# Kernel tuning notes

Hardware: AMD Instinct MI355X
Metric: run time of the kernel (lower is better)

Reference implementation:

```python
import jax, jax.numpy as jnp
import numpy as np

B, S, D, H, DH = 2, 2048, 1024, 16, 64
GLOBAL_RATIO = 0.1
LN_EPS = 1e-5


def setup_inputs() -> dict:
    key = jax.random.key(0)
    ks = jax.random.split(key, 8)
    w = lambda k, shape: jax.random.normal(k, shape, jnp.float32) * 0.02
    return {
        'x': jax.random.normal(ks[0], (B, S, D), jnp.float32),
        'Wq': w(ks[1], (D, H * DH)),
        'Wk': w(ks[2], (D, H * DH)),
        'Wv': w(ks[3], (D, H * DH)),
        'Wo': w(ks[4], (H * DH, D)),
        'bo': jnp.zeros((D,), jnp.float32),
        'ln_gamma': jnp.ones((DH,), jnp.float32),
        'ln_beta': jnp.zeros((DH,), jnp.float32),
        'Wg': w(ks[5], (2 * DH, DH)),
        'bg': jnp.zeros((DH,), jnp.float32),
    }


def _layernorm(x, gamma, beta):
    mu = jnp.mean(x, axis=-1, keepdims=True)
    var = jnp.mean(jnp.square(x - mu), axis=-1, keepdims=True)
    return (x - mu) * jax.lax.rsqrt(var + LN_EPS) * gamma + beta


def reference(x, Wq, Wk, Wv, Wo, bo, ln_gamma, ln_beta, Wg, bg):
    b, s, _ = x.shape
    # projections -> [b, h, n, d]
    split = lambda t: t.reshape(b, s, H, DH).transpose(0, 2, 1, 3)
    q = split(x @ Wq)
    k = split(x @ Wk)
    v = split(x @ Wv)
    scale = DH ** -0.5

    # local (full) attention: manual QK^T / softmax / AV
    scores = jnp.einsum('bhnd,bhmd->bhnm', q, k) * scale  # [b,h,s,s]
    attn = jax.nn.softmax(scores, axis=-1)
    local_out = jnp.einsum('bhnm,bhmd->bhnd', attn, v)

    # cross-segment fusion: top-k keys by norm per (b, h)
    num_global = max(1, int(s * GLOBAL_RATIO))
    key_norms = jnp.linalg.norm(k, axis=-1)  # [b,h,s]
    _, top_idx = jax.lax.top_k(key_norms, num_global)  # [b,h,g]
    idx = top_idx[..., None]  # [b,h,g,1]
    global_k = jnp.take_along_axis(k, idx, axis=2)  # [b,h,g,d]
    global_v = jnp.take_along_axis(v, idx, axis=2)
    g_scores = jnp.einsum('bhnd,bhgd->bhng', q, global_k) * scale
    g_attn = jax.nn.softmax(g_scores, axis=-1)
    global_out = jnp.einsum('bhng,bhgd->bhnd', g_attn, global_v)
    global_out = _layernorm(global_out, ln_gamma, ln_beta)

    # learned gate over [local, global]
    cat = jnp.concatenate([local_out, global_out], axis=-1)  # [b,h,s,2d]
    gate = jax.nn.sigmoid(cat @ Wg + bg)
    fused = gate * local_out + (1.0 - gate) * global_out

    out = fused.transpose(0, 2, 1, 3).reshape(b, s, H * DH)  # b h n d -> b n (h d)
    return out @ Wo + bo
```

## Files before the change

### kernel.cpp

```cpp
#include <hip/hip_runtime.h>


constexpr int SEQ    = 2048;
constexpr int DMODEL = 1024;
constexpr int NH     = 16;
constexpr int DHEAD  = 64;
constexpr int BHT    = 32;
constexpr int NG     = 204;
constexpr int NGPAD  = 256;
constexpr float LNEPS = 1e-5f;

typedef __attribute__((ext_vector_type(8))) short short8;
typedef __attribute__((ext_vector_type(4))) short short4v;
typedef __attribute__((ext_vector_type(4))) float f32x4;

__device__ __forceinline__ unsigned short f2bf(float f) {
    unsigned int u = __float_as_uint(f);
    u += 0x7FFFu + ((u >> 16) & 1u);
    return (unsigned short)(u >> 16);
}
__device__ __forceinline__ float bf2f(unsigned short b) {
    return __uint_as_float(((unsigned int)b) << 16);
}

__global__ __launch_bounds__(256)
void prep_k(const float* __restrict__ x,
            const float* __restrict__ Wq, const float* __restrict__ Wv,
            const float* __restrict__ Wo, const float* __restrict__ Wk,
            const float* __restrict__ Wg,
            unsigned short* __restrict__ xh, unsigned short* __restrict__ xl,
            unsigned short* __restrict__ Wqt, unsigned short* __restrict__ Wvt,
            unsigned short* __restrict__ Wot, unsigned short* __restrict__ Wkh,
            unsigned short* __restrict__ Wkl, unsigned short* __restrict__ Wgt)
{
    const int bid = blockIdx.x;
    const int tid = threadIdx.x;

    if (bid < 2048) {
        int i = (bid * 256 + tid) << 3;
        short8 h, l;
#pragma unroll
        for (int j = 0; j < 8; ++j) {
            float v = x[i + j];
            unsigned short hb = f2bf(v);
            h[j] = (short)hb;
            l[j] = (short)f2bf(v - bf2f(hb));
        }
        *(short8*)(xh + i) = h;
        *(short8*)(xl + i) = l;
        return;
    }
    if (bid == 3072) {
#pragma unroll
        for (int i = 0; i < 32; ++i) {
            int o = tid * 32 + i;
            int dg = o >> 7, jj = o & 127;
            Wgt[o] = f2bf(Wg[jj * 64 + dg]);
        }
        return;
    }

    __shared__ float tile[64][68];
    const int sub = bid - 2048;
    const int which = sub >> 8;
    const int b = sub & 255;
    const int n0 = (b & 15) * 64, k0 = (b >> 4) * 64;
    const float* W = (which == 0) ? Wq : (which == 1) ? Wv : (which == 2) ? Wo : Wk;
    const int Kd = DMODEL, Nd = DMODEL;

#pragma unroll
    for (int p = 0; p < 4; ++p) {
        int c = tid + (p << 8);
        int r = c >> 4, c4 = (c & 15) << 2;
        *(float4*)&tile[r][c4] = *(const float4*)(W + (size_t)(k0 + r) * Nd + n0 + c4);
    }
    __syncthreads();
#pragma unroll
    for (int p = 0; p < 4; ++p) {
        int c = tid + (p << 8);
        int n = c >> 4, k4 = (c & 15) << 2;
        if (which < 3) {
            unsigned short* Wt = (which == 0) ? Wqt : (which == 1) ? Wvt : Wot;
            short4v o;
#pragma unroll
            for (int j = 0; j < 4; ++j) o[j] = (short)f2bf(tile[k4 + j][n]);
            *(short4v*)(Wt + (size_t)(n0 + n) * Kd + k0 + k4) = o;
        } else {
            short4v oh, ol;
#pragma unroll
            for (int j = 0; j < 4; ++j) {
                float v = tile[k4 + j][n];
                unsigned short hb = f2bf(v);
                oh[j] = (short)hb;
                ol[j] = (short)f2bf(v - bf2f(hb));
            }
            *(short4v*)(Wkh + (size_t)(n0 + n) * Kd + k0 + k4) = oh;
            *(short4v*)(Wkl + (size_t)(n0 + n) * Kd + k0 + k4) = ol;
        }
    }
}

__global__ __launch_bounds__(512)
void gemm_bf16_k(const unsigned short* __restrict__ A,
                 const unsigned short* __restrict__ Bt,
                 const float* __restrict__ bias,
                 void* __restrict__ outv, void* __restrict__ outv2,
                 unsigned short* __restrict__ vtout,
                 int M, int N, int K, int mode)
{
    __shared__ __align__(16) unsigned short As[128][72];
    __shared__ __align__(16) unsigned short Bs[128][72];
    const int tid = threadIdx.x;
    const int lane = tid & 63, wave = tid >> 6;
    const int quad = lane >> 4, ln = lane & 15;
    const int mh = (wave >> 2) << 6;
    const int nh = (wave & 3) << 5;
    const int m0 = blockIdx.y * 128, n0 = blockIdx.x * 128;

    f32x4 acc[4][2];
#pragma unroll
    for (int i = 0; i < 4; ++i)
#pragma unroll
        for (int j = 0; j < 2; ++j) acc[i][j] = (f32x4){0.f, 0.f, 0.f, 0.f};

    short8 areg[2], breg[2];
#pragma unroll
    for (int p = 0; p < 2; ++p) {
        int c = tid + (p << 9);
        int row = c >> 3, col8 = (c & 7) << 3;
        areg[p] = *(const short8*)(A + (size_t)(m0 + row) * K + col8);
        breg[p] = *(const short8*)(Bt + (size_t)(n0 + row) * K + col8);
    }

    for (int k0 = 0; k0 < K; k0 += 64) {
        __syncthreads();
#pragma unroll
        for (int p = 0; p < 2; ++p) {
            int c = tid + (p << 9);
            int row = c >> 3, col8 = (c & 7) << 3;
            *(short8*)&As[row][col8] = areg[p];
            *(short8*)&Bs[row][col8] = breg[p];
        }
        __syncthreads();
        if (k0 + 64 < K) {
#pragma unroll
            for (int p = 0; p < 2; ++p) {
                int c = tid + (p << 9);
                int row = c >> 3, col8 = (c & 7) << 3;
                areg[p] = *(const short8*)(A + (size_t)(m0 + row) * K + k0 + 64 + col8);
                breg[p] = *(const short8*)(Bt + (size_t)(n0 + row) * K + k0 + 64 + col8);
            }
        }
#pragma unroll
        for (int ch = 0; ch < 2; ++ch) {
            short8 af[4], bf[2];
#pragma unroll
            for (int mt = 0; mt < 4; ++mt)
                af[mt] = *(const short8*)&As[mh + mt * 16 + ln][ch * 32 + quad * 8];
#pragma unroll
            for (int nt = 0; nt < 2; ++nt)
                bf[nt] = *(const short8*)&Bs[nh + nt * 16 + ln][ch * 32 + quad * 8];
#pragma unroll
            for (int mt = 0; mt < 4; ++mt)
#pragma unroll
                for (int nt = 0; nt < 2; ++nt)
                    acc[mt][nt] = __builtin_amdgcn_mfma_f32_16x16x32_bf16(
                        af[mt], bf[nt], acc[mt][nt], 0, 0, 0);
        }
    }

    if (mode == 0) {
        float* out = (float*)outv;
#pragma unroll
        for (int mt = 0; mt < 4; ++mt)
#pragma unroll
            for (int nt = 0; nt < 2; ++nt)
#pragma unroll
                for (int r = 0; r < 4; ++r) {
                    int m = m0 + mh + mt * 16 + quad * 4 + r;
                    int n = n0 + nh + nt * 16 + ln;
                    out[(size_t)m * N + n] = acc[mt][nt][r] + bias[n];
                }
    } else {
#pragma unroll
        for (int mt = 0; mt < 4; ++mt)
#pragma unroll
            for (int nt = 0; nt < 2; ++nt) {
                int n = n0 + nh + nt * 16 + ln;
                int mb = m0 + mh + mt * 16 + quad * 4;
                int b = mb >> 11, s0 = mb & (SEQ - 1);
                int d = n & 63;
                if (n < DMODEL) {
                    int h = n >> 6;
                    unsigned short* qp_ =
                        (unsigned short*)outv + ((size_t)(b * NH + h) * SEQ + s0) * DHEAD + d;
#pragma unroll
                    for (int r = 0; r < 4; ++r)
                        qp_[(size_t)r * DHEAD] = f2bf(acc[mt][nt][r] * 0.125f);
                } else {
                    int h = (n >> 6) - NH;
                    unsigned short* vp_ =
                        (unsigned short*)outv2 + ((size_t)(b * NH + h) * SEQ + s0) * DHEAD + d;
                    short4v tv;
#pragma unroll
                    for (int r = 0; r < 4; ++r) {
                        unsigned short bv = f2bf(acc[mt][nt][r]);
                        vp_[(size_t)r * DHEAD] = bv;
                        tv[r] = (short)bv;
                    }
                    *(short4v*)(vtout + ((size_t)(b * NH + h) * DHEAD + d) * SEQ + s0) = tv;
                }
            }
    }
}

__global__ __launch_bounds__(512)
void gemm_kproj_mfma(const unsigned short* __restrict__ xh,
                     const unsigned short* __restrict__ xl,
                     const unsigned short* __restrict__ Wh,
                     const unsigned short* __restrict__ Wl,
                     unsigned short* __restrict__ kout,
                     float* __restrict__ norms2)
{
    __shared__ __align__(16) unsigned short Ah[64][72];
    __shared__ __align__(16) unsigned short Al[64][72];
    __shared__ __align__(16) unsigned short Bh[128][72];
    __shared__ __align__(16) unsigned short Bl[128][72];
    const int K = DMODEL;
    const int tid = threadIdx.x;
    const int lane = tid & 63, wave = tid >> 6;
    const int quad = lane >> 4, ln = lane & 15;
    const int mh = (wave >> 1) << 4;
    const int nh = (wave & 1) << 6;
    const int m0 = blockIdx.y * 64, n0 = blockIdx.x * 128;

    f32x4 acc[4];
#pragma unroll
    for (int j = 0; j < 4; ++j) acc[j] = (f32x4){0.f, 0.f, 0.f, 0.f};

    const int arow = tid >> 3, acol8 = (tid & 7) << 3;
    short8 ahreg, alreg, bhreg[2], blreg[2];
    {
        size_t ga = (size_t)(m0 + arow) * K + acol8;
        ahreg = *(const short8*)(xh + ga);
        alreg = *(const short8*)(xl + ga);
#pragma unroll
        for (int p = 0; p < 2; ++p) {
            int c = tid + (p << 9);
            int row = c >> 3, col8 = (c & 7) << 3;
            size_t gb = (size_t)(n0 + row) * K + col8;
            bhreg[p] = *(const short8*)(Wh + gb);
            blreg[p] = *(const short8*)(Wl + gb);
        }
    }

    for (int k0 = 0; k0 < K; k0 += 64) {
        __syncthreads();
        *(short8*)&Ah[arow][acol8] = ahreg;
        *(short8*)&Al[arow][acol8] = alreg;
#pragma unroll
        for (int p = 0; p < 2; ++p) {
            int c = tid + (p << 9);
            int row = c >> 3, col8 = (c & 7) << 3;
            *(short8*)&Bh[row][col8] = bhreg[p];
            *(short8*)&Bl[row][col8] = blreg[p];
        }
        __syncthreads();
        if (k0 + 64 < K) {
            size_t ga = (size_t)(m0 + arow) * K + k0 + 64 + acol8;
            ahreg = *(const short8*)(xh + ga);
            alreg = *(const short8*)(xl + ga);
#pragma unroll
            for (int p = 0; p < 2; ++p) {
                int c = tid + (p << 9);
                int row = c >> 3, col8 = (c & 7) << 3;
                size_t gb = (size_t)(n0 + row) * K + k0 + 64 + col8;
                bhreg[p] = *(const short8*)(Wh + gb);
                blreg[p] = *(const short8*)(Wl + gb);
            }
        }
#pragma unroll
        for (int ch = 0; ch < 2; ++ch) {
            short8 bh4[4], bl4[4];
#pragma unroll
            for (int nt = 0; nt < 4; ++nt) {
                bh4[nt] = *(const short8*)&Bh[nh + nt * 16 + ln][ch * 32 + quad * 8];
                bl4[nt] = *(const short8*)&Bl[nh + nt * 16 + ln][ch * 32 + quad * 8];
            }
            short8 ah = *(const short8*)&Ah[mh + ln][ch * 32 + quad * 8];
            short8 al = *(const short8*)&Al[mh + ln][ch * 32 + quad * 8];
#pragma unroll
            for (int nt = 0; nt < 4; ++nt) {
                acc[nt] = __builtin_amdgcn_mfma_f32_16x16x32_bf16(ah, bh4[nt], acc[nt], 0, 0, 0);
                acc[nt] = __builtin_amdgcn_mfma_f32_16x16x32_bf16(ah, bl4[nt], acc[nt], 0, 0, 0);
                acc[nt] = __builtin_amdgcn_mfma_f32_16x16x32_bf16(al, bh4[nt], acc[nt], 0, 0, 0);
            }
        }
    }

    const int h = (n0 + nh) >> 6;
#pragma unroll
    for (int r = 0; r < 4; ++r) {
        int m = m0 + mh + quad * 4 + r;
        int b = m >> 11, s = m & (SEQ - 1);
        size_t rowbase = ((size_t)(b * NH + h) * SEQ + s) * DHEAD;
#pragma unroll
        for (int nt = 0; nt < 4; ++nt)
            kout[rowbase + nt * 16 + ln] = f2bf(acc[nt][r]);
        float s2 = acc[0][r] * acc[0][r] + acc[1][r] * acc[1][r] +
                   acc[2][r] * acc[2][r] + acc[3][r] * acc[3][r];
#pragma unroll
        for (int off = 1; off <= 8; off <<= 1)
            s2 += __shfl_xor(s2, off);
        if (ln == 0)
            norms2[(size_t)(b * NH + h) * SEQ + s] = s2;
    }
}

__global__ __launch_bounds__(512)
void topk_gather_k(const float* __restrict__ norms2,
                   const unsigned short* __restrict__ k,
                   const unsigned short* __restrict__ v,
                   unsigned short* __restrict__ gk,
                   unsigned short* __restrict__ gvt)
{
    __shared__ unsigned long long keys[SEQ];
    __shared__ int tix[NGPAD];
    __shared__ __align__(16) unsigned short T[64][72];
    const int bh = blockIdx.x;
    const int tid = threadIdx.x;
    const float* nb = norms2 + (size_t)bh * SEQ;
    const size_t base = (size_t)bh * SEQ * DHEAD;

    for (int i = tid; i < SEQ; i += 512) {
        float nrm = sqrtf(nb[i]);
        keys[i] = ((unsigned long long)__float_as_uint(nrm) << 32) |
                  (unsigned int)(0xFFFFFFFFu - (unsigned int)i);
    }
    __syncthreads();
    for (int kk = 2; kk <= SEQ; kk <<= 1) {
        for (int j = kk >> 1; j > 0; j >>= 1) {
            for (int i = tid; i < SEQ; i += 512) {
                int ixj = i ^ j;
                if (ixj > i) {
                    unsigned long long a = keys[i], b = keys[ixj];
                    bool up = ((i & kk) == 0);
                    if ((a > b) == up) { keys[i] = b; keys[ixj] = a; }
                }
            }
            __syncthreads();
        }
    }
    if (tid < NGPAD) {
        tix[tid] = (tid < NG)
            ? (int)(0xFFFFFFFFu - (unsigned int)(keys[SEQ - 1 - tid] & 0xFFFFFFFFu))
            : 0;
    }
    __syncthreads();

    for (int t = 0; t < NGPAD / 64; ++t) {
        {
            int idx = tid;
            int row = idx >> 3, col8 = (idx & 7) << 3;
            int g = t * 64 + row;
            short8 kv = (short8)0, vv = (short8)0;
            if (g < NG) {
                int sidx = tix[g];
                kv = *(const short8*)(k + base + (size_t)sidx * DHEAD + col8);
                vv = *(const short8*)(v + base + (size_t)sidx * DHEAD + col8);
            }
            *(short8*)(gk + ((size_t)bh * NGPAD + g) * DHEAD + col8) = kv;
            *(short8*)&T[row][col8] = vv;
        }
        __syncthreads();
        {
            int idx = tid;
            int d = idx >> 3, k8 = (idx & 7) << 3;
            short8 o;
#pragma unroll
            for (int i = 0; i < 8; ++i) o[i] = (short)T[k8 + i][d];
            *(short8*)(gvt + ((size_t)bh * DHEAD + d) * NGPAD + t * 64 + k8) = o;
        }
        __syncthreads();
    }
}

__global__ __launch_bounds__(512)
void attn_fused_k(const unsigned short* __restrict__ qb,
                  const unsigned short* __restrict__ kb,
                  const unsigned short* __restrict__ vt,
                  const unsigned short* __restrict__ gk,
                  const unsigned short* __restrict__ gvt,
                  const unsigned short* __restrict__ Wgt,
                  const float* __restrict__ gamma,
                  const float* __restrict__ beta,
                  const float* __restrict__ bg,
                  unsigned short* __restrict__ fused)
{
    __shared__ __align__(16) unsigned short Ks[64][72];
    __shared__ __align__(16) unsigned short Vt[64][72];
    __shared__ __align__(16) unsigned short Ps[128][72];
    __shared__ __align__(16) unsigned short Wgs[64][136];
    const int flat = blockIdx.x;
    const int bh = ((flat >> 7) << 3) | (flat & 7);
    const int q0 = ((flat >> 3) & 15) * 128;
    const int tid = threadIdx.x;
    const int lane = tid & 63, wave = tid >> 6;
    const int quad = lane >> 4, ln = lane & 15;
    const size_t base = (size_t)bh * SEQ * DHEAD;
    const unsigned short* gkb = gk + (size_t)bh * NGPAD * DHEAD;
    const unsigned short* gvb = gvt + (size_t)bh * DHEAD * NGPAD;

#pragma unroll
    for (int p = 0; p < 2; ++p) {
        int idx = tid + (p << 9);
        *(short8*)&Wgs[idx >> 4][(idx & 15) << 3] = *(const short8*)(Wgt + idx * 8);
    }

    short8 qf0, qf1;
    {
        const unsigned short* qp = qb + base + (size_t)(q0 + wave * 16 + ln) * DHEAD;
        qf0 = *(const short8*)(qp + quad * 8);
        qf1 = *(const short8*)(qp + 32 + quad * 8);
    }

    f32x4 O[4], Og[4];
#pragma unroll
    for (int nt = 0; nt < 4; ++nt) {
        O[nt] = (f32x4){0.f, 0.f, 0.f, 0.f};
        Og[nt] = (f32x4){0.f, 0.f, 0.f, 0.f};
    }
    float ls[4] = {0.f, 0.f, 0.f, 0.f};
    float lg[4] = {0.f, 0.f, 0.f, 0.f};

    short8 kreg = *(const short8*)(kb + base + (size_t)(tid >> 3) * DHEAD + ((tid & 7) << 3));
    short8 vreg = *(const short8*)(vt + base + (size_t)(tid >> 3) * SEQ + ((tid & 7) << 3));
    const int srow = tid >> 3, scol8 = (tid & 7) << 3;

    for (int t = 0; t < SEQ / 64; ++t) {
        __syncthreads();
        *(short8*)&Ks[srow][scol8] = kreg;
        *(short8*)&Vt[srow][scol8] = vreg;
        __syncthreads();
        if (t + 1 < SEQ / 64) {
            kreg = *(const short8*)(kb + base + (size_t)((t + 1) * 64 + srow) * DHEAD + scol8);
            vreg = *(const short8*)(vt + base + (size_t)srow * SEQ + (t + 1) * 64 + scol8);
        } else {
            kreg = *(const short8*)(gkb + (size_t)srow * DHEAD + scol8);
            vreg = *(const short8*)(gvb + (size_t)srow * NGPAD + scol8);
        }

        f32x4 s[4];
#pragma unroll
        for (int nt = 0; nt < 4; ++nt) {
            s[nt] = (f32x4){0.f, 0.f, 0.f, 0.f};
            short8 kf0 = *(const short8*)&Ks[nt * 16 + ln][quad * 8];
            short8 kf1 = *(const short8*)&Ks[nt * 16 + ln][32 + quad * 8];
            s[nt] = __builtin_amdgcn_mfma_f32_16x16x32_bf16(qf0, kf0, s[nt], 0, 0, 0);
            s[nt] = __builtin_amdgcn_mfma_f32_16x16x32_bf16(qf1, kf1, s[nt], 0, 0, 0);
        }
#pragma unroll
        for (int nt = 0; nt < 4; ++nt)
#pragma unroll
            for (int r = 0; r < 4; ++r) {
                float p = __expf(s[nt][r]);
                unsigned int us = __float_as_uint(p) >> 16;
                Ps[wave * 16 + quad * 4 + r][nt * 16 + ln] = (unsigned short)us;
                ls[r] += __uint_as_float(us << 16);
            }
#pragma unroll
        for (int ch = 0; ch < 2; ++ch) {
            short8 pf = *(const short8*)&Ps[wave * 16 + ln][ch * 32 + quad * 8];
#pragma unroll
            for (int nt = 0; nt < 4; ++nt) {
                short8 vf = *(const short8*)&Vt[nt * 16 + ln][ch * 32 + quad * 8];
                O[nt] = __builtin_amdgcn_mfma_f32_16x16x32_bf16(pf, vf, O[nt], 0, 0, 0);
            }
        }
    }

    for (int t = 0; t < NGPAD / 64; ++t) {
        __syncthreads();
        *(short8*)&Ks[srow][scol8] = kreg;
        *(short8*)&Vt[srow][scol8] = vreg;
        __syncthreads();
        if (t + 1 < NGPAD / 64) {
            kreg = *(const short8*)(gkb + (size_t)((t + 1) * 64 + srow) * DHEAD + scol8);
            vreg = *(const short8*)(gvb + (size_t)srow * NGPAD + (t + 1) * 64 + scol8);
        }

        f32x4 s[4];
#pragma unroll
        for (int nt = 0; nt < 4; ++nt) {
            s[nt] = (f32x4){0.f, 0.f, 0.f, 0.f};
            short8 kf0 = *(const short8*)&Ks[nt * 16 + ln][quad * 8];
            short8 kf1 = *(const short8*)&Ks[nt * 16 + ln][32 + quad * 8];
            s[nt] = __builtin_amdgcn_mfma_f32_16x16x32_bf16(qf0, kf0, s[nt], 0, 0, 0);
            s[nt] = __builtin_amdgcn_mfma_f32_16x16x32_bf16(qf1, kf1, s[nt], 0, 0, 0);
        }
#pragma unroll
        for (int nt = 0; nt < 4; ++nt) {
            bool valid = (t * 64 + nt * 16 + ln) < NG;
#pragma unroll
            for (int r = 0; r < 4; ++r) {
                float p = valid ? __expf(s[nt][r]) : 0.f;
                unsigned int us = __float_as_uint(p) >> 16;
                Ps[wave * 16 + quad * 4 + r][nt * 16 + ln] = (unsigned short)us;
                lg[r] += __uint_as_float(us << 16);
            }
        }
#pragma unroll
        for (int ch = 0; ch < 2; ++ch) {
            short8 pf = *(const short8*)&Ps[wave * 16 + ln][ch * 32 + quad * 8];
#pragma unroll
            for (int nt = 0; nt < 4; ++nt) {
                short8 vf = *(const short8*)&Vt[nt * 16 + ln][ch * 32 + quad * 8];
                Og[nt] = __builtin_amdgcn_mfma_f32_16x16x32_bf16(pf, vf, Og[nt], 0, 0, 0);
            }
        }
    }

#pragma unroll
    for (int off = 1; off <= 8; off <<= 1)
#pragma unroll
        for (int r = 0; r < 4; ++r) {
            ls[r] += __shfl_xor(ls[r], off);
            lg[r] += __shfl_xor(lg[r], off);
        }
    float invl[4];
#pragma unroll
    for (int r = 0; r < 4; ++r) invl[r] = 1.f / ls[r];

    float xs[4][4];
#pragma unroll
    for (int r = 0; r < 4; ++r) {
        float inv = 1.f / lg[r];
#pragma unroll
        for (int nt = 0; nt < 4; ++nt) xs[nt][r] = Og[nt][r] * inv;
    }
    float mu[4], rsd[4];
#pragma unroll
    for (int r = 0; r < 4; ++r) {
        float sm = xs[0][r] + xs[1][r] + xs[2][r] + xs[3][r];
#pragma unroll
        for (int off = 1; off <= 8; off <<= 1) sm += __shfl_xor(sm, off);
        mu[r] = sm * (1.f / 64.f);
    }
#pragma unroll
    for (int r = 0; r < 4; ++r) {
        float sv = 0.f;
#pragma unroll
        for (int nt = 0; nt < 4; ++nt) {
            float d = xs[nt][r] - mu[r];
            sv += d * d;
        }
#pragma unroll
        for (int off = 1; off <= 8; off <<= 1) sv += __shfl_xor(sv, off);
        rsd[r] = rsqrtf(sv * (1.f / 64.f) + LNEPS);
    }
#pragma unroll
    for (int nt = 0; nt < 4; ++nt) {
        float g = gamma[nt * 16 + ln], bb = beta[nt * 16 + ln];
#pragma unroll
        for (int r = 0; r < 4; ++r)
            xs[nt][r] = (xs[nt][r] - mu[r]) * rsd[r] * g + bb;
    }

    float lf[4][4];
#pragma unroll
    for (int nt = 0; nt < 4; ++nt)
#pragma unroll
        for (int r = 0; r < 4; ++r) {
            lf[nt][r] = O[nt][r] * invl[r];
            Ps[wave * 16 + quad * 4 + r][nt * 16 + ln] = f2bf(lf[nt][r]);
        }
    f32x4 gacc[4];
#pragma unroll
    for (int ng = 0; ng < 4; ++ng) {
        float bgv = bg[ng * 16 + ln];
        gacc[ng] = (f32x4){bgv, bgv, bgv, bgv};
    }
#pragma unroll
    for (int ch = 0; ch < 2; ++ch) {
        short8 af = *(const short8*)&Ps[wave * 16 + ln][ch * 32 + quad * 8];
#pragma unroll
        for (int ng = 0; ng < 4; ++ng) {
            short8 bf = *(const short8*)&Wgs[ng * 16 + ln][ch * 32 + quad * 8];
            gacc[ng] = __builtin_amdgcn_mfma_f32_16x16x32_bf16(af, bf, gacc[ng], 0, 0, 0);
        }
    }
#pragma unroll
    for (int nt = 0; nt < 4; ++nt)
#pragma unroll
        for (int r = 0; r < 4; ++r)
            Ps[wave * 16 + quad * 4 + r][nt * 16 + ln] = f2bf(xs[nt][r]);
#pragma unroll
    for (int ch = 0; ch < 2; ++ch) {
        short8 af = *(const short8*)&Ps[wave * 16 + ln][ch * 32 + quad * 8];
#pragma unroll
        for (int ng = 0; ng < 4; ++ng) {
            short8 bf = *(const short8*)&Wgs[ng * 16 + ln][64 + ch * 32 + quad * 8];
            gacc[ng] = __builtin_amdgcn_mfma_f32_16x16x32_bf16(af, bf, gacc[ng], 0, 0, 0);
        }
    }

    const int b = bh >> 4, h = bh & 15;
#pragma unroll
    for (int ng = 0; ng < 4; ++ng)
#pragma unroll
        for (int r = 0; r < 4; ++r) {
            float gt = 1.f / (1.f + __expf(-gacc[ng][r]));
            float f = gt * lf[ng][r] + (1.f - gt) * xs[ng][r];
            int s = q0 + wave * 16 + quad * 4 + r;
            fused[((size_t)(b * SEQ + s)) * DMODEL + h * DHEAD + ng * 16 + ln] = f2bf(f);
        }
}

extern "C" void kernel_launch(void* const* d_in, const int* in_sizes, int n_in,
                              void* d_out, int out_size, void* d_ws, size_t ws_size,
                              hipStream_t stream)
{
    (void)in_sizes; (void)n_in; (void)out_size; (void)ws_size;
    const float* x    = (const float*)d_in[0];
    const float* Wq   = (const float*)d_in[1];
    const float* Wk   = (const float*)d_in[2];
    const float* Wv   = (const float*)d_in[3];
    const float* Wo   = (const float*)d_in[4];
    const float* bo   = (const float*)d_in[5];
    const float* ln_g = (const float*)d_in[6];
    const float* ln_b = (const float*)d_in[7];
    const float* Wg   = (const float*)d_in[8];
    const float* bg   = (const float*)d_in[9];

    char* w = (char*)d_ws;
    const size_t MB = 1024ull * 1024ull;
    unsigned short* kb16  = (unsigned short*)(w);
    unsigned short* qb16  = (unsigned short*)(w + 8 * MB);
    unsigned short* vb16  = (unsigned short*)(w + 16 * MB);
    unsigned short* vt16  = (unsigned short*)(w + 24 * MB);
    unsigned short* xh    = (unsigned short*)(w + 32 * MB);
    unsigned short* xl    = (unsigned short*)(w + 40 * MB);
    unsigned short* Wqt   = (unsigned short*)(w + 48 * MB);
    unsigned short* Wvt   = (unsigned short*)(w + 50 * MB);
    unsigned short* Wot   = (unsigned short*)(w + 52 * MB);
    unsigned short* Wkh   = (unsigned short*)(w + 54 * MB);
    unsigned short* Wkl   = (unsigned short*)(w + 56 * MB);
    unsigned short* Wgt   = (unsigned short*)(w + 58 * MB);
    float*          norms2= (float*)(w + 59 * MB);
    unsigned short* gk16  = (unsigned short*)(w + 60 * MB);
    unsigned short* gvt16 = (unsigned short*)(w + 61 * MB);
    unsigned short* fusedb = xh;

    const int M = 4096, N = 1024, K = 1024;

    prep_k<<<3073, 256, 0, stream>>>(x, Wq, Wv, Wo, Wk, Wg,
                                     xh, xl, Wqt, Wvt, Wot, Wkh, Wkl, Wgt);

    dim3 gqv(2048 / 128, M / 128);
    gemm_bf16_k<<<gqv, 512, 0, stream>>>(xh, Wqt, nullptr, qb16, vb16, vt16,
                                         M, 2048, K, 3);

    dim3 gkp(N / 128, M / 64);
    gemm_kproj_mfma<<<gkp, 512, 0, stream>>>(xh, xl, Wkh, Wkl, kb16, norms2);

    topk_gather_k<<<BHT, 512, 0, stream>>>(norms2, kb16, vb16, gk16, gvt16);

    attn_fused_k<<<512, 512, 0, stream>>>(qb16, kb16, vt16, gk16, gvt16, Wgt,
                                          ln_g, ln_b, bg, fusedb);

    dim3 go_(N / 128, M / 128);
    gemm_bf16_k<<<go_, 512, 0, stream>>>(fusedb, Wot, bo, (float*)d_out, nullptr,
                                         nullptr, M, N, K, 0);
}
```

Measured before the change: 295.6 us.

## Double-buffer K/V tiles, merge local/global loops, fold log2e into Q scale

The K and V shared-memory tiles become double-buffered, so each iteration needs one barrier instead of two, and the next tile's global load overlaps the current tile's MFMA work. The local and global attention loops are merged into one loop with a uniform branch that picks the accumulator. The Q projection scale now includes log2(e), so the softmax can use exp2f instead of __expf, removing a multiply per score. The cost is about twice the K/V LDS footprint and a bit more branching in the merged loop.

```diff
diff --git a/kernel.cpp b/kernel.cpp
--- a/kernel.cpp
+++ b/kernel.cpp
@@ -9,6 +9,7 @@
 constexpr int NG     = 204;
 constexpr int NGPAD  = 256;
 constexpr float LNEPS = 1e-5f;
+constexpr float QSCALE = 0.18033688011112042f;
 
 typedef __attribute__((ext_vector_type(8))) short short8;
 typedef __attribute__((ext_vector_type(4))) short short4v;
@@ -196,7 +197,7 @@
                         (unsigned short*)outv + ((size_t)(b * NH + h) * SEQ + s0) * DHEAD + d;
 #pragma unroll
                     for (int r = 0; r < 4; ++r)
-                        qp_[(size_t)r * DHEAD] = f2bf(acc[mt][nt][r] * 0.125f);
+                        qp_[(size_t)r * DHEAD] = f2bf(acc[mt][nt][r] * QSCALE);
                 } else {
                     int h = (n >> 6) - NH;
                     unsigned short* vp_ =
@@ -397,8 +398,8 @@
                   const float* __restrict__ bg,
                   unsigned short* __restrict__ fused)
 {
-    __shared__ __align__(16) unsigned short Ks[64][72];
-    __shared__ __align__(16) unsigned short Vt[64][72];
+    __shared__ __align__(16) unsigned short Ks[2][64][72];
+    __shared__ __align__(16) unsigned short Vt[2][64][72];
     __shared__ __align__(16) unsigned short Ps[128][72];
     __shared__ __align__(16) unsigned short Wgs[64][136];
     const int flat = blockIdx.x;
@@ -410,6 +411,8 @@
     const size_t base = (size_t)bh * SEQ * DHEAD;
     const unsigned short* gkb = gk + (size_t)bh * NGPAD * DHEAD;
     const unsigned short* gvb = gvt + (size_t)bh * DHEAD * NGPAD;
+    const int srow = tid >> 3, scol8 = (tid & 7) << 3;
+    const int NT = SEQ / 64 + NGPAD / 64;
 
 #pragma unroll
     for (int p = 0; p < 2; ++p) {
@@ -433,90 +436,79 @@
     float ls[4] = {0.f, 0.f, 0.f, 0.f};
     float lg[4] = {0.f, 0.f, 0.f, 0.f};
 
-    short8 kreg = *(const short8*)(kb + base + (size_t)(tid >> 3) * DHEAD + ((tid & 7) << 3));
-    short8 vreg = *(const short8*)(vt + base + (size_t)(tid >> 3) * SEQ + ((tid & 7) << 3));
-    const int srow = tid >> 3, scol8 = (tid & 7) << 3;
-
-    for (int t = 0; t < SEQ / 64; ++t) {
+    auto load_tile = [&](int tt, short8& kr, short8& vr) {
+        if (tt < SEQ / 64) {
+            kr = *(const short8*)(kb + base + (size_t)(tt * 64 + srow) * DHEAD + scol8);
+            vr = *(const short8*)(vt + base + (size_t)srow * SEQ + tt * 64 + scol8);
+        } else {
+            int tg = tt - SEQ / 64;
+            kr = *(const short8*)(gkb + (size_t)(tg * 64 + srow) * DHEAD + scol8);
+            vr = *(const short8*)(gvb + (size_t)srow * NGPAD + tg * 64 + scol8);
+        }
+    };
+
+    short8 kreg, vreg;
+    load_tile(0, kreg, vreg);
+    *(short8*)&Ks[0][srow][scol8] = kreg;
+    *(short8*)&Vt[0][srow][scol8] = vreg;
+
+    for (int t = 0; t < NT; ++t) {
+        const int cur = t & 1;
+        const bool isglob = (t >= SEQ / 64);
+        if (t + 1 < NT) load_tile(t + 1, kreg, vreg);
         __syncthreads();
-        *(short8*)&Ks[srow][scol8] = kreg;
-        *(short8*)&Vt[srow][scol8] = vreg;
-        __syncthreads();
-        if (t + 1 < SEQ / 64) {
-            kreg = *(const short8*)(kb + base + (size_t)((t + 1) * 64 + srow) * DHEAD + scol8);
-            vreg = *(const short8*)(vt + base + (size_t)srow * SEQ + (t + 1) * 64 + scol8);
-        } else {
-            kreg = *(const short8*)(gkb + (size_t)srow * DHEAD + scol8);
-            vreg = *(const short8*)(gvb + (size_t)srow * NGPAD + scol8);
-        }
 
         f32x4 s[4];
 #pragma unroll
         for (int nt = 0; nt < 4; ++nt) {
             s[nt] = (f32x4){0.f, 0.f, 0.f, 0.f};
-            short8 kf0 = *(const short8*)&Ks[nt * 16 + ln][quad * 8];
-            short8 kf1 = *(const short8*)&Ks[nt * 16 + ln][32 + quad * 8];
+            short8 kf0 = *(const short8*)&Ks[cur][nt * 16 + ln][quad * 8];
+            short8 kf1 = *(const short8*)&Ks[cur][nt * 16 + ln][32 + quad * 8];
             s[nt] = __builtin_amdgcn_mfma_f32_16x16x32_bf16(qf0, kf0, s[nt], 0, 0, 0);
             s[nt] = __builtin_amdgcn_mfma_f32_16x16x32_bf16(qf1, kf1, s[nt], 0, 0, 0);
         }
-#pragma unroll
-        for (int nt = 0; nt < 4; ++nt)
-#pragma unroll
-            for (int r = 0; r < 4; ++r) {
-                float p = __expf(s[nt][r]);
-                unsigned int us = __float_as_uint(p) >> 16;
-                Ps[wave * 16 + quad * 4 + r][nt * 16 + ln] = (unsigned short)us;
-                ls[r] += __uint_as_float(us << 16);
-            }
+
+        if (!isglob) {
+#pragma unroll
+            for (int nt = 0; nt < 4; ++nt)
+#pragma unroll
+                for (int r = 0; r < 4; ++r) {
+                    float p = exp2f(s[nt][r]);
+                    unsigned int us = __float_as_uint(p) >> 16;
+                    Ps[wave * 16 + quad * 4 + r][nt * 16 + ln] = (unsigned short)us;
+                    ls[r] += __uint_as_float(us << 16);
+                }
+        } else {
+            int tg64 = (t - SEQ / 64) * 64;
+#pragma unroll
+            for (int nt = 0; nt < 4; ++nt) {
+                bool valid = (tg64 + nt * 16 + ln) < NG;
+#pragma unroll
+                for (int r = 0; r < 4; ++r) {
+                    float p = valid ? exp2f(s[nt][r]) : 0.f;
+                    unsigned int us = __float_as_uint(p) >> 16;
+                    Ps[wave * 16 + quad * 4 + r][nt * 16 + ln] = (unsigned short)us;
+                    lg[r] += __uint_as_float(us << 16);
+                }
+            }
+        }
+
 #pragma unroll
         for (int ch = 0; ch < 2; ++ch) {
             short8 pf = *(const short8*)&Ps[wave * 16 + ln][ch * 32 + quad * 8];
 #pragma unroll
             for (int nt = 0; nt < 4; ++nt) {
-                short8 vf = *(const short8*)&Vt[nt * 16 + ln][ch * 32 + quad * 8];
-                O[nt] = __builtin_amdgcn_mfma_f32_16x16x32_bf16(pf, vf, O[nt], 0, 0, 0);
-            }
-        }
-    }
-
-    for (int t = 0; t < NGPAD / 64; ++t) {
-        __syncthreads();
-        *(short8*)&Ks[srow][scol8] = kreg;
-        *(short8*)&Vt[srow][scol8] = vreg;
-        __syncthreads();
-        if (t + 1 < NGPAD / 64) {
-            kreg = *(const short8*)(gkb + (size_t)((t + 1) * 64 + srow) * DHEAD + scol8);
-            vreg = *(const short8*)(gvb + (size_t)srow * NGPAD + (t + 1) * 64 + scol8);
-        }
-
-        f32x4 s[4];
-#pragma unroll
-        for (int nt = 0; nt < 4; ++nt) {
-            s[nt] = (f32x4){0.f, 0.f, 0.f, 0.f};
-            short8 kf0 = *(const short8*)&Ks[nt * 16 + ln][quad * 8];
-            short8 kf1 = *(const short8*)&Ks[nt * 16 + ln][32 + quad * 8];
-            s[nt] = __builtin_amdgcn_mfma_f32_16x16x32_bf16(qf0, kf0, s[nt], 0, 0, 0);
-            s[nt] = __builtin_amdgcn_mfma_f32_16x16x32_bf16(qf1, kf1, s[nt], 0, 0, 0);
-        }
-#pragma unroll
-        for (int nt = 0; nt < 4; ++nt) {
-            bool valid = (t * 64 + nt * 16 + ln) < NG;
-#pragma unroll
-            for (int r = 0; r < 4; ++r) {
-                float p = valid ? __expf(s[nt][r]) : 0.f;
-                unsigned int us = __float_as_uint(p) >> 16;
-                Ps[wave * 16 + quad * 4 + r][nt * 16 + ln] = (unsigned short)us;
-                lg[r] += __uint_as_float(us << 16);
-            }
-        }
-#pragma unroll
-        for (int ch = 0; ch < 2; ++ch) {
-            short8 pf = *(const short8*)&Ps[wave * 16 + ln][ch * 32 + quad * 8];
-#pragma unroll
-            for (int nt = 0; nt < 4; ++nt) {
-                short8 vf = *(const short8*)&Vt[nt * 16 + ln][ch * 32 + quad * 8];
-                Og[nt] = __builtin_amdgcn_mfma_f32_16x16x32_bf16(pf, vf, Og[nt], 0, 0, 0);
-            }
+                short8 vf = *(const short8*)&Vt[cur][nt * 16 + ln][ch * 32 + quad * 8];
+                if (!isglob)
+                    O[nt] = __builtin_amdgcn_mfma_f32_16x16x32_bf16(pf, vf, O[nt], 0, 0, 0);
+                else
+                    Og[nt] = __builtin_amdgcn_mfma_f32_16x16x32_bf16(pf, vf, Og[nt], 0, 0, 0);
+            }
+        }
+
+        if (t + 1 < NT) {
+            *(short8*)&Ks[cur ^ 1][srow][scol8] = kreg;
+            *(short8*)&Vt[cur ^ 1][srow][scol8] = vreg;
         }
     }
 
```

Result: slower. 368.7 us (+24.8%).
